# Performance work log

Hardware: AMD Instinct MI355X
Metric: run time of the kernel (lower is better)

Reference implementation:

```python
import jax, jax.numpy as jnp
import numpy as np

N = 100000
E = 1600000
F_IN = 128
H = 256
C = 40
BN_EPS = 1e-5


def setup_inputs() -> dict:
    key = jax.random.key(0)
    ks = jax.random.split(key, 16)
    x = jax.random.normal(ks[0], (N, F_IN), dtype=jnp.float32)
    edge_index = jax.random.randint(ks[1], (2, E), 0, N, dtype=jnp.int64)
    # pre layer
    pre_w = jax.random.normal(ks[2], (H, F_IN), dtype=jnp.float32) * (1.0 / np.sqrt(F_IN))
    pre_b = jnp.zeros((H,), jnp.float32)
    # batchnorm params stacked [5, 4, H]: gamma, beta, running_mean, running_var
    gamma = jnp.ones((5, H), jnp.float32)
    beta = jnp.zeros((5, H), jnp.float32)
    rmean = jax.random.normal(ks[3], (5, H), dtype=jnp.float32) * 0.1
    rvar = jax.random.uniform(ks[4], (5, H), dtype=jnp.float32) * 0.5 + 0.5
    bn_params = jnp.stack([gamma, beta, rmean, rvar], axis=1)  # [5,4,H]
    # 3 SAGEConv layers: lin_l (neighbor, with bias), lin_r (root, no bias)
    s = 1.0 / np.sqrt(H)
    lin_l_w = jax.random.normal(ks[5], (3, H, H), dtype=jnp.float32) * s
    lin_l_b = jnp.zeros((3, H), jnp.float32)
    lin_r_w = jax.random.normal(ks[6], (3, H, H), dtype=jnp.float32) * s
    # post layers
    post1_w = jax.random.normal(ks[7], (H, H), dtype=jnp.float32) * s
    post1_b = jnp.zeros((H,), jnp.float32)
    post2_w = jax.random.normal(ks[8], (C, H), dtype=jnp.float32) * s
    post2_b = jnp.zeros((C,), jnp.float32)
    return {
        "x": x, "edge_index": edge_index,
        "pre_w": pre_w, "pre_b": pre_b, "bn_params": bn_params,
        "lin_l_w": lin_l_w, "lin_l_b": lin_l_b, "lin_r_w": lin_r_w,
        "post1_w": post1_w, "post1_b": post1_b,
        "post2_w": post2_w, "post2_b": post2_b,
    }


def _bn(x, p):
    # eval-mode BatchNorm1d with running stats; p: [4, H]
    g, b, m, v = p[0], p[1], p[2], p[3]
    return (x - m) * (g * jax.lax.rsqrt(v + BN_EPS)) + b


def _sage_conv(x, src, dst, wl, bl, wr):
    # PyG SAGEConv (aggr='mean'): lin_l(mean_{j in N(i)} x_j) + lin_r(x_i)
    msg = x[src]                                             # [E, H] gather
    agg = jax.ops.segment_sum(msg, dst, num_segments=N)       # [N, H] scatter
    cnt = jax.ops.segment_sum(jnp.ones((src.shape[0],), x.dtype), dst, num_segments=N)
    mean = agg / jnp.maximum(cnt, 1.0)[:, None]
    return mean @ wl.T + bl + x @ wr.T


def reference(x, edge_index, pre_w, pre_b, bn_params, lin_l_w, lin_l_b, lin_r_w,
              post1_w, post1_b, post2_w, post2_b):
    src, dst = edge_index[0], edge_index[1]
    h = x @ pre_w.T + pre_b
    h = jax.nn.relu(_bn(h, bn_params[0]))  # dropout is identity in eval mode
    for i in range(3):
        h = _sage_conv(h, src, dst, lin_l_w[i], lin_l_b[i], lin_r_w[i])
        h = jax.nn.relu(_bn(h, bn_params[i + 1]))
    h = h @ post1_w.T + post1_b
    h = jax.nn.relu(_bn(h, bn_params[4]))
    logits = h @ post2_w.T + post2_b
    return jax.nn.log_softmax(logits, axis=1)
```

## Files before the change

kernel.cpp:

```cpp
#include <hip/hip_runtime.h>
#include <cstdint>
#include <cstddef>

#define N_NODES 100000
#define N_EDGES 1600000
#define F_INDIM 128
#define HDIM 256
#define C_OUT 40
#define BN_EPS 1e-5f

typedef unsigned short bf16_t;
typedef __attribute__((ext_vector_type(8))) short bf16x8;
typedef __attribute__((ext_vector_type(4))) float f32x4;

__device__ __forceinline__ float bf2f(unsigned int u) {
  return __uint_as_float(u << 16);
}
__device__ __forceinline__ bf16_t f2bf(float f) {
  unsigned int x = __float_as_uint(f);
  return (bf16_t)((x + 0x7fffu + ((x >> 16) & 1u)) >> 16);
}

__global__ void k_cvt(const float* __restrict__ s, bf16_t* __restrict__ d, int n) {
  int i = (blockIdx.x * blockDim.x + threadIdx.x) * 4;
  if (i >= n) return;
  float4 v = *reinterpret_cast<const float4*>(&s[i]);
  uint2 o;
  o.x = (unsigned)f2bf(v.x) | ((unsigned)f2bf(v.y) << 16);
  o.y = (unsigned)f2bf(v.z) | ((unsigned)f2bf(v.w) << 16);
  *reinterpret_cast<uint2*>(&d[i]) = o;
}

__global__ void k_rank(const int* __restrict__ dst, int* __restrict__ cursor,
                       int* __restrict__ rank, int E) {
  for (int e = blockIdx.x * blockDim.x + threadIdx.x; e < E; e += gridDim.x * blockDim.x)
    rank[e] = atomicAdd(&cursor[dst[e]], 1);
}

__global__ __launch_bounds__(1024)
void k_scan_local(const int* __restrict__ cnt, int* __restrict__ row_ptr,
                  int* __restrict__ blk_sum, int n) {
  __shared__ int buf[1024];
  int tid = threadIdx.x;
  int i = blockIdx.x * 1024 + tid;
  int v = (i < n) ? cnt[i] : 0;
  buf[tid] = v;
  __syncthreads();
  for (int off = 1; off < 1024; off <<= 1) {
    int t = (tid >= off) ? buf[tid - off] : 0;
    __syncthreads();
    buf[tid] += t;
    __syncthreads();
  }
  if (i < n) row_ptr[i] = buf[tid] - v;
  if (tid == 1023) blk_sum[blockIdx.x] = buf[1023];
}

__global__ __launch_bounds__(128)
void k_scan_blk(const int* __restrict__ blk_sum, int* __restrict__ blk_off, int nb) {
  __shared__ int buf[128];
  int tid = threadIdx.x;
  int v = (tid < nb) ? blk_sum[tid] : 0;
  buf[tid] = v;
  __syncthreads();
  for (int off = 1; off < 128; off <<= 1) {
    int t = (tid >= off) ? buf[tid - off] : 0;
    __syncthreads();
    buf[tid] += t;
    __syncthreads();
  }
  if (tid < nb) blk_off[tid] = buf[tid] - v;
}

__global__ void k_scan_add(int* __restrict__ row_ptr, const int* __restrict__ blk_off, int n) {
  int i = blockIdx.x * blockDim.x + threadIdx.x;
  if (i < n) row_ptr[i] += blk_off[i >> 10];
  if (i == 0) row_ptr[n] = N_EDGES;
}

__global__ void k_place(const int* __restrict__ src, const int* __restrict__ dst,
                        const int* __restrict__ rank, const int* __restrict__ row_ptr,
                        int* __restrict__ csr, int E) {
  for (int e = blockIdx.x * blockDim.x + threadIdx.x; e < E; e += gridDim.x * blockDim.x)
    csr[row_ptr[dst[e]] + rank[e]] = src[e];
}

__global__ void k_inv(const int* __restrict__ cnt, float* __restrict__ inv, int n) {
  int i = blockIdx.x * blockDim.x + threadIdx.x;
  if (i < n) inv[i] = 1.0f / (float)(cnt[i] > 0 ? cnt[i] : 1);
}

__device__ __forceinline__ void add8(float* acc, uint4 r) {
  acc[0] += bf2f(r.x & 0xffffu); acc[1] += bf2f(r.x >> 16);
  acc[2] += bf2f(r.y & 0xffffu); acc[3] += bf2f(r.y >> 16);
  acc[4] += bf2f(r.z & 0xffffu); acc[5] += bf2f(r.z >> 16);
  acc[6] += bf2f(r.w & 0xffffu); acc[7] += bf2f(r.w >> 16);
}

__global__ __launch_bounds__(256)
void k_aggregate(const bf16_t* __restrict__ h, const int* __restrict__ row_ptr,
                 const int* __restrict__ csr, const float* __restrict__ inv_deg,
                 bf16_t* __restrict__ mean) {
  int w = threadIdx.x >> 6, lane = threadIdx.x & 63;
  int node = blockIdx.x * 4 + w;
  if (node >= N_NODES) return;
  int beg = row_ptr[node], end = row_ptr[node + 1];
  int half = lane >> 5;
  int l32 = lane & 31;
  float acc[8] = {};
  int deg = end - beg;
  int p = beg;
  int p8 = beg + (deg & ~7);
  for (; p < p8; p += 8) {
    int s0 = csr[p + half];
    int s1 = csr[p + 2 + half];
    int s2 = csr[p + 4 + half];
    int s3 = csr[p + 6 + half];
    uint4 r0 = *reinterpret_cast<const uint4*>(&h[(size_t)s0 * HDIM + l32 * 8]);
    uint4 r1 = *reinterpret_cast<const uint4*>(&h[(size_t)s1 * HDIM + l32 * 8]);
    uint4 r2 = *reinterpret_cast<const uint4*>(&h[(size_t)s2 * HDIM + l32 * 8]);
    uint4 r3 = *reinterpret_cast<const uint4*>(&h[(size_t)s3 * HDIM + l32 * 8]);
    add8(acc, r0);
    add8(acc, r1);
    add8(acc, r2);
    add8(acc, r3);
  }
  if (end - p >= 4) {
    int s0 = csr[p + half];
    int s1 = csr[p + 2 + half];
    uint4 r0 = *reinterpret_cast<const uint4*>(&h[(size_t)s0 * HDIM + l32 * 8]);
    uint4 r1 = *reinterpret_cast<const uint4*>(&h[(size_t)s1 * HDIM + l32 * 8]);
    add8(acc, r0);
    add8(acc, r1);
    p += 4;
  }
  for (; p < end; p += 2) {
    int e = p + half;
    if (e < end) {
      int s = csr[e];
      uint4 r = *reinterpret_cast<const uint4*>(&h[(size_t)s * HDIM + l32 * 8]);
      add8(acc, r);
    }
  }
#pragma unroll
  for (int k = 0; k < 8; ++k) acc[k] += __shfl_xor(acc[k], 32);
  if (half == 0) {
    float iv = inv_deg[node];
    uint4 o;
    o.x = (unsigned)f2bf(acc[0] * iv) | ((unsigned)f2bf(acc[1] * iv) << 16);
    o.y = (unsigned)f2bf(acc[2] * iv) | ((unsigned)f2bf(acc[3] * iv) << 16);
    o.z = (unsigned)f2bf(acc[4] * iv) | ((unsigned)f2bf(acc[5] * iv) << 16);
    o.w = (unsigned)f2bf(acc[6] * iv) | ((unsigned)f2bf(acc[7] * iv) << 16);
    *reinterpret_cast<uint4*>(&mean[(size_t)node * HDIM + l32 * 8]) = o;
  }
}

__device__ __forceinline__ void store1(float* p, float v) { *p = v; }
__device__ __forceinline__ void store1(bf16_t* p, float v) { *p = f2bf(v); }

template <typename TOUT>
__global__ __launch_bounds__(256)
void gemm_mfma(const bf16_t* __restrict__ A0, const bf16_t* __restrict__ W0,
               const bf16_t* __restrict__ A1, const bf16_t* __restrict__ W1,
               const float* __restrict__ bias, const float* __restrict__ bn,
               TOUT* __restrict__ C, int M, int K, int OUT, int dual) {
  __shared__ bf16_t lds[2][2][128 * 32];
  const int tid = threadIdx.x;
  const int lane = tid & 63, wid = tid >> 6;
  const int wm = wid >> 1, wn = wid & 1;
  const int row0 = blockIdx.x * 128, col0 = blockIdx.y * 128;
  const int l15 = lane & 15, l4 = lane >> 4;

  const int nk = K / 32;
  const int nsteps = dual ? nk * 2 : nk;

  f32x4 acc[4][4] = {};

  const int srow_base = wid * 32 + (lane >> 2);
  const int skk = (lane & 3) * 8;

  auto stage = [&](int s, int b) {
    const bf16_t* A = (s < nk) ? A0 : A1;
    const bf16_t* W = (s < nk) ? W0 : W1;
    int kk0 = ((s < nk) ? s : s - nk) * 32 + skk;
#pragma unroll
    for (int c = 0; c < 2; ++c) {
      int chunk = wid * 2 + c;
      int row = srow_base + c * 16;
      int ar = row0 + row; if (ar >= M) ar = M - 1;
      int br = col0 + row; if (br >= OUT) br = OUT - 1;
      const bf16_t* gA = &A[(size_t)ar * K + kk0];
      const bf16_t* gB = &W[(size_t)br * K + kk0];
      __builtin_amdgcn_global_load_lds(
          (const __attribute__((address_space(1))) unsigned int*)gA,
          (__attribute__((address_space(3))) unsigned int*)&lds[b][0][chunk * 512],
          16, 0, 0);
      __builtin_amdgcn_global_load_lds(
          (const __attribute__((address_space(1))) unsigned int*)gB,
          (__attribute__((address_space(3))) unsigned int*)&lds[b][1][chunk * 512],
          16, 0, 0);
    }
  };

  stage(0, 0);
  __syncthreads();
  int cur = 0;
  for (int s = 0; s < nsteps; ++s) {
    if (s + 1 < nsteps) stage(s + 1, cur ^ 1);
    const bf16_t* pa = &lds[cur][0][l15 * 32 + l4 * 8];
    const bf16_t* pb = &lds[cur][1][l15 * 32 + l4 * 8];
    bf16x8 a[4], b[4];
#pragma unroll
    for (int i = 0; i < 4; ++i)
      a[i] = *reinterpret_cast<const bf16x8*>(&pa[(wm * 64 + i * 16) * 32]);
#pragma unroll
    for (int j = 0; j < 4; ++j)
      b[j] = *reinterpret_cast<const bf16x8*>(&pb[(wn * 64 + j * 16) * 32]);
#pragma unroll
    for (int i = 0; i < 4; ++i)
#pragma unroll
      for (int j = 0; j < 4; ++j)
        acc[i][j] = __builtin_amdgcn_mfma_f32_16x16x32_bf16(a[i], b[j], acc[i][j], 0, 0, 0);
    if (s + 1 < nsteps) {
      __syncthreads();
      cur ^= 1;
    }
  }

#pragma unroll
  for (int j = 0; j < 4; ++j) {
    int col = col0 + wn * 64 + j * 16 + l15;
    if (col >= OUT) continue;
    float bs = bias ? bias[col] : 0.f;
    float scale = 1.f, shift = bs;
    bool has_bn = (bn != nullptr);
    if (has_bn) {
      float g = bn[col], bb = bn[256 + col], mm = bn[512 + col], vv = bn[768 + col];
      float is = g * rsqrtf(vv + BN_EPS);
      scale = is; shift = (bs - mm) * is + bb;
    }
#pragma unroll
    for (int i = 0; i < 4; ++i) {
#pragma unroll
      for (int r = 0; r < 4; ++r) {
        int row = row0 + wm * 64 + i * 16 + l4 * 4 + r;
        if (row >= M) continue;
        float v = acc[i][j][r];
        v = has_bn ? fmaxf(v * scale + shift, 0.f) : (v + bs);
        store1(&C[(size_t)row * OUT + col], v);
      }
    }
  }
}

__global__ __launch_bounds__(256)
void k_logsoftmax(const float* __restrict__ logits, float* __restrict__ out, int M) {
  int row = blockIdx.x * 4 + (threadIdx.x >> 6);
  if (row >= M) return;
  int lane = threadIdx.x & 63;
  float v = (lane < C_OUT) ? logits[(size_t)row * C_OUT + lane] : -1e30f;
  float m = v;
#pragma unroll
  for (int o = 32; o; o >>= 1) m = fmaxf(m, __shfl_xor(m, o));
  float e = (lane < C_OUT) ? expf(v - m) : 0.f;
  float s = e;
#pragma unroll
  for (int o = 32; o; o >>= 1) s += __shfl_xor(s, o);
  if (lane < C_OUT) out[(size_t)row * C_OUT + lane] = v - m - logf(s);
}

extern "C" void kernel_launch(void* const* d_in, const int* in_sizes, int n_in,
                              void* d_out, int out_size, void* d_ws, size_t ws_size,
                              hipStream_t stream) {
  const float* x       = (const float*)d_in[0];
  const int*   ei      = (const int*)d_in[1];
  const float* pre_w   = (const float*)d_in[2];
  const float* pre_b   = (const float*)d_in[3];
  const float* bn      = (const float*)d_in[4];
  const float* lin_l_w = (const float*)d_in[5];
  const float* lin_l_b = (const float*)d_in[6];
  const float* lin_r_w = (const float*)d_in[7];
  const float* post1_w = (const float*)d_in[8];
  const float* post1_b = (const float*)d_in[9];
  const float* post2_w = (const float*)d_in[10];
  const float* post2_b = (const float*)d_in[11];
  float* out = (float*)d_out;

  const int* src = ei;
  const int* dstv = ei + N_EDGES;

  char* base = (char*)d_ws;
  size_t off = 0;
  auto alloc = [&](size_t bytes) -> void* {
    void* p = base + off;
    off = (off + bytes + 255) & ~(size_t)255;
    return p;
  };
  bf16_t* hA = (bf16_t*)alloc((size_t)N_NODES * HDIM * 2);
  bf16_t* hB = (bf16_t*)alloc((size_t)N_NODES * HDIM * 2);
  bf16_t* hC = (bf16_t*)alloc((size_t)N_NODES * HDIM * 2);
  int* row_ptr = (int*)alloc((size_t)(N_NODES + 1) * 4);
  int* cursor  = (int*)alloc((size_t)N_NODES * 4);
  int* csr     = (int*)alloc((size_t)N_EDGES * 4);
  int* rank    = (int*)alloc((size_t)N_EDGES * 4);
  float* inv   = (float*)alloc((size_t)N_NODES * 4);
  int* blk_sum = (int*)alloc(128 * 4);
  int* blk_off = (int*)alloc(128 * 4);
  bf16_t* w_pre = (bf16_t*)alloc((size_t)HDIM * F_INDIM * 2);
  bf16_t* w_ll  = (bf16_t*)alloc((size_t)3 * HDIM * HDIM * 2);
  bf16_t* w_lr  = (bf16_t*)alloc((size_t)3 * HDIM * HDIM * 2);
  bf16_t* w_p1  = (bf16_t*)alloc((size_t)HDIM * HDIM * 2);
  bf16_t* w_p2  = (bf16_t*)alloc((size_t)C_OUT * HDIM * 2);
  (void)n_in; (void)in_sizes; (void)out_size;
  if (off > ws_size) return;

  bf16_t* x_bf = hB;

  {
    int n;
    n = N_NODES * F_INDIM;
    k_cvt<<<(n / 4 + 255) / 256, 256, 0, stream>>>(x, x_bf, n);
    n = HDIM * F_INDIM;
    k_cvt<<<(n / 4 + 255) / 256, 256, 0, stream>>>(pre_w, w_pre, n);
    n = 3 * HDIM * HDIM;
    k_cvt<<<(n / 4 + 255) / 256, 256, 0, stream>>>(lin_l_w, w_ll, n);
    k_cvt<<<(n / 4 + 255) / 256, 256, 0, stream>>>(lin_r_w, w_lr, n);
    n = HDIM * HDIM;
    k_cvt<<<(n / 4 + 255) / 256, 256, 0, stream>>>(post1_w, w_p1, n);
    n = C_OUT * HDIM;
    k_cvt<<<(n / 4 + 255) / 256, 256, 0, stream>>>(post2_w, w_p2, n);
  }

  hipMemsetAsync(cursor, 0, (size_t)N_NODES * 4, stream);
  k_rank<<<2048, 256, 0, stream>>>(dstv, cursor, rank, N_EDGES);
  int nb = (N_NODES + 1023) / 1024;
  k_scan_local<<<nb, 1024, 0, stream>>>(cursor, row_ptr, blk_sum, N_NODES);
  k_scan_blk<<<1, 128, 0, stream>>>(blk_sum, blk_off, nb);
  k_scan_add<<<(N_NODES + 255) / 256, 256, 0, stream>>>(row_ptr, blk_off, N_NODES);
  k_place<<<2048, 256, 0, stream>>>(src, dstv, rank, row_ptr, csr, N_EDGES);
  k_inv<<<(N_NODES + 255) / 256, 256, 0, stream>>>(cursor, inv, N_NODES);

  dim3 gH((N_NODES + 127) / 128, 2);
  gemm_mfma<bf16_t><<<gH, 256, 0, stream>>>(
      x_bf, w_pre, nullptr, nullptr, pre_b, bn, hA, N_NODES, F_INDIM, HDIM, 0);

  bf16_t* hcur = hA;
  bf16_t* hnext = hC;
  for (int i = 0; i < 3; ++i) {
    k_aggregate<<<N_NODES / 4, 256, 0, stream>>>(hcur, row_ptr, csr, inv, hB);
    gemm_mfma<bf16_t><<<gH, 256, 0, stream>>>(
        hB, w_ll + (size_t)i * HDIM * HDIM,
        hcur, w_lr + (size_t)i * HDIM * HDIM,
        lin_l_b + (size_t)i * HDIM,
        bn + (size_t)(i + 1) * 4 * HDIM,
        hnext, N_NODES, HDIM, HDIM, 1);
    bf16_t* t = hcur; hcur = hnext; hnext = t;
  }
  gemm_mfma<bf16_t><<<gH, 256, 0, stream>>>(
      hcur, w_p1, nullptr, nullptr, post1_b,
      bn + (size_t)4 * 4 * HDIM, hnext, N_NODES, HDIM, HDIM, 0);
  float* logits = (float*)hB;
  dim3 gC((N_NODES + 127) / 128, 1);
  gemm_mfma<float><<<gC, 256, 0, stream>>>(
      hnext, w_p2, nullptr, nullptr, post2_b,
      nullptr, logits, N_NODES, HDIM, C_OUT, 0);
  k_logsoftmax<<<(N_NODES + 3) / 4, 256, 0, stream>>>(logits, out, N_NODES);
}
```

Baseline: 794.0 us.

## Widen GEMM tile to cover all 256 output columns per block

The MFMA GEMM tile grows from 128x128 to 128x256, so each block computes every output column and the grid's second dimension is removed. The A operand (activations) is then read from global memory once instead of twice. The cost is double the accumulator registers (32 f32x4 per thread), larger LDS for B, and possibly lower occupancy. The C=40 GEMM now stages 256 weight rows, mostly clamped duplicates, so it does wasted MFMA work on that layer.

```diff
diff --git a/kernel.cpp b/kernel.cpp
--- a/kernel.cpp
+++ b/kernel.cpp
@@ -164,19 +164,20 @@
                const bf16_t* __restrict__ A1, const bf16_t* __restrict__ W1,
                const float* __restrict__ bias, const float* __restrict__ bn,
                TOUT* __restrict__ C, int M, int K, int OUT, int dual) {
-  __shared__ bf16_t lds[2][2][128 * 32];
+  __shared__ bf16_t ldsA[2][128 * 32];
+  __shared__ bf16_t ldsB[2][256 * 32];
   const int tid = threadIdx.x;
   const int lane = tid & 63, wid = tid >> 6;
   const int wm = wid >> 1, wn = wid & 1;
-  const int row0 = blockIdx.x * 128, col0 = blockIdx.y * 128;
+  const int row0 = blockIdx.x * 128;
   const int l15 = lane & 15, l4 = lane >> 4;
 
   const int nk = K / 32;
   const int nsteps = dual ? nk * 2 : nk;
 
-  f32x4 acc[4][4] = {};
-
-  const int srow_base = wid * 32 + (lane >> 2);
+  f32x4 acc[4][8] = {};
+
+  const int srow = lane >> 2;
   const int skk = (lane & 3) * 8;
 
   auto stage = [&](int s, int b) {
@@ -186,18 +187,19 @@
 #pragma unroll
     for (int c = 0; c < 2; ++c) {
       int chunk = wid * 2 + c;
-      int row = srow_base + c * 16;
-      int ar = row0 + row; if (ar >= M) ar = M - 1;
-      int br = col0 + row; if (br >= OUT) br = OUT - 1;
-      const bf16_t* gA = &A[(size_t)ar * K + kk0];
-      const bf16_t* gB = &W[(size_t)br * K + kk0];
+      int ar = row0 + chunk * 16 + srow; if (ar >= M) ar = M - 1;
       __builtin_amdgcn_global_load_lds(
-          (const __attribute__((address_space(1))) unsigned int*)gA,
-          (__attribute__((address_space(3))) unsigned int*)&lds[b][0][chunk * 512],
+          (const __attribute__((address_space(1))) unsigned int*)&A[(size_t)ar * K + kk0],
+          (__attribute__((address_space(3))) unsigned int*)&ldsA[b][chunk * 512],
           16, 0, 0);
+    }
+#pragma unroll
+    for (int c = 0; c < 4; ++c) {
+      int chunk = wid * 4 + c;
+      int br = chunk * 16 + srow; if (br >= OUT) br = OUT - 1;
       __builtin_amdgcn_global_load_lds(
-          (const __attribute__((address_space(1))) unsigned int*)gB,
-          (__attribute__((address_space(3))) unsigned int*)&lds[b][1][chunk * 512],
+          (const __attribute__((address_space(1))) unsigned int*)&W[(size_t)br * K + kk0],
+          (__attribute__((address_space(3))) unsigned int*)&ldsB[b][chunk * 512],
           16, 0, 0);
     }
   };
@@ -207,19 +209,19 @@
   int cur = 0;
   for (int s = 0; s < nsteps; ++s) {
     if (s + 1 < nsteps) stage(s + 1, cur ^ 1);
-    const bf16_t* pa = &lds[cur][0][l15 * 32 + l4 * 8];
-    const bf16_t* pb = &lds[cur][1][l15 * 32 + l4 * 8];
-    bf16x8 a[4], b[4];
+    const bf16_t* pa = &ldsA[cur][l15 * 32 + l4 * 8];
+    const bf16_t* pb = &ldsB[cur][l15 * 32 + l4 * 8];
+    bf16x8 a[4], b[8];
 #pragma unroll
     for (int i = 0; i < 4; ++i)
       a[i] = *reinterpret_cast<const bf16x8*>(&pa[(wm * 64 + i * 16) * 32]);
 #pragma unroll
-    for (int j = 0; j < 4; ++j)
-      b[j] = *reinterpret_cast<const bf16x8*>(&pb[(wn * 64 + j * 16) * 32]);
+    for (int j = 0; j < 8; ++j)
+      b[j] = *reinterpret_cast<const bf16x8*>(&pb[(wn * 128 + j * 16) * 32]);
 #pragma unroll
     for (int i = 0; i < 4; ++i)
 #pragma unroll
-      for (int j = 0; j < 4; ++j)
+      for (int j = 0; j < 8; ++j)
         acc[i][j] = __builtin_amdgcn_mfma_f32_16x16x32_bf16(a[i], b[j], acc[i][j], 0, 0, 0);
     if (s + 1 < nsteps) {
       __syncthreads();
@@ -228,8 +230,8 @@
   }
 
 #pragma unroll
-  for (int j = 0; j < 4; ++j) {
-    int col = col0 + wn * 64 + j * 16 + l15;
+  for (int j = 0; j < 8; ++j) {
+    int col = wn * 128 + j * 16 + l15;
     if (col >= OUT) continue;
     float bs = bias ? bias[col] : 0.f;
     float scale = 1.f, shift = bs;
@@ -340,7 +342,7 @@
   k_place<<<2048, 256, 0, stream>>>(src, dstv, rank, row_ptr, csr, N_EDGES);
   k_inv<<<(N_NODES + 255) / 256, 256, 0, stream>>>(cursor, inv, N_NODES);
 
-  dim3 gH((N_NODES + 127) / 128, 2);
+  dim3 gH((N_NODES + 127) / 128, 1);
   gemm_mfma<bf16_t><<<gH, 256, 0, stream>>>(
       x_bf, w_pre, nullptr, nullptr, pre_b, bn, hA, N_NODES, F_INDIM, HDIM, 0);
 
@@ -360,8 +362,7 @@
       hcur, w_p1, nullptr, nullptr, post1_b,
       bn + (size_t)4 * 4 * HDIM, hnext, N_NODES, HDIM, HDIM, 0);
   float* logits = (float*)hB;
-  dim3 gC((N_NODES + 127) / 128, 1);
-  gemm_mfma<float><<<gC, 256, 0, stream>>>(
+  gemm_mfma<float><<<gH, 256, 0, stream>>>(
       hnext, w_p2, nullptr, nullptr, post2_b,
       nullptr, logits, N_NODES, HDIM, C_OUT, 0);
   k_logsoftmax<<<(N_NODES + 3) / 4, 256, 0, stream>>>(logits, out, N_NODES);
```

Measured after the change: 1.133 ms. +42.7%, slower.
